# Performance work log

Hardware: AMD Instinct MI355X
Metric: run time of the kernel (lower is better)

## Reference

```python
import jax, jax.numpy as jnp
import numpy as np

SIZE = 8192
NB = 64            # nr_blocks
BS = SIZE // NB    # block_size = 128
NTOK = 4096


def setup_inputs() -> dict:
    key = jax.random.key(0)
    k1, k2, k3, k4 = jax.random.split(key, 4)
    # kaiming_normal on [nb, bs, bs]: fan_in per torch default for 3D is bs*bs? torch
    # kaiming_normal_ uses fan_in = bs (last dim sizes); we just use std=sqrt(2/BS).
    std = np.sqrt(2.0 / BS).astype(np.float32)
    x = jax.random.normal(k1, (NTOK, SIZE), dtype=jnp.float32)
    w1 = jax.random.normal(k2, (NB, BS, BS), dtype=jnp.float32) * std
    w2 = jax.random.normal(k3, (NB, BS, BS), dtype=jnp.float32) * std
    bias = jax.random.uniform(k4, (SIZE,), dtype=jnp.float32, minval=-1.0, maxval=1.0) * np.sqrt(1.0 / SIZE).astype(np.float32)
    return {"x": x, "w1": w1, "w2": w2, "bias": bias}


def _monarch(x, w1, w2, bias):
    B = x.reshape(-1, SIZE).shape[0]
    z = x.reshape(B, NB, BS)
    # first block-diagonal matmul: per-block [B,BS] @ [BS,BS]
    h = jnp.einsum('bkc,kcd->bkd', z, w1)            # [B, NB, BS]
    # Permute(size, NB): (B, NB, BS) -> (B, BS, NB) flattened
    h = h.transpose(0, 2, 1).reshape(B, NB, BS)      # regroup into NB blocks of BS
    # second block-diagonal matmul
    h = jnp.einsum('bkc,kcd->bkd', h, w2)            # [B, NB, BS]
    # Permute(size, BS): reshape (B, BS, NB) -> transpose -> (B, NB, BS)
    h = h.reshape(B, BS, NB).transpose(0, 2, 1)
    return h.reshape(x.shape) + bias


def reference(x, w1, w2, bias):
    return _monarch(x, w1, w2, bias)
```

## Files before the change

kernel.cpp:

```cpp
#include <hip/hip_runtime.h>

#define SZ 8192
#define WT_BYTES ((size_t)128 * 16384 * 2)

typedef short short8 __attribute__((ext_vector_type(8)));
typedef float f32x4 __attribute__((ext_vector_type(4)));

static __device__ __forceinline__ unsigned short f2bf(float f){
    unsigned u = __float_as_uint(f);
    u += 0x7fffu + ((u >> 16) & 1u);
    return (unsigned short)(u >> 16);
}

__global__ __launch_bounds__(256) void Monarch_prep(const float* __restrict__ w1,
                                                    const float* __restrict__ w2,
                                                    unsigned short* __restrict__ wt)
{
    __shared__ unsigned short T[128][132];
    int blk = blockIdx.x;
    const float* src = (blk < 64) ? (w1 + (size_t)blk * 16384)
                                  : (w2 + (size_t)(blk - 64) * 16384);
    unsigned short* dst = wt + (size_t)blk * 16384;
    int i  = threadIdx.x;
    int cs = i >> 5;
    int p0 = (i & 31) * 4;
    for (int rr = 0; rr < 16; ++rr){
        int c = rr * 8 + cs;
        f32x4 v = *(const f32x4*)(src + c * 128 + p0);
        T[p0 + 0][c] = f2bf(v[0]);
        T[p0 + 1][c] = f2bf(v[1]);
        T[p0 + 2][c] = f2bf(v[2]);
        T[p0 + 3][c] = f2bf(v[3]);
    }
    __syncthreads();
    for (int rr = 0; rr < 16; ++rr){
        int d = rr * 8 + cs;
        ushort4 o;
        o.x = T[d][p0 + 0]; o.y = T[d][p0 + 1]; o.z = T[d][p0 + 2]; o.w = T[d][p0 + 3];
        *(ushort4*)(dst + d * 128 + p0) = o;
    }
}

__global__ __launch_bounds__(512, 4) void Monarch_main(const float* __restrict__ x,
                                                       const unsigned short* __restrict__ w1T,
                                                       const unsigned short* __restrict__ w2T,
                                                       const float* __restrict__ bias,
                                                       float* __restrict__ out)
{
    __shared__ __align__(16) unsigned short s[16 * 2048];

    int b     = blockIdx.x;
    int xcd   = b & 7;
    int local = b >> 3;
    int g     = local & 3;
    int tile  = (xcd << 5) | (local >> 2);
    int t0    = tile << 4;
    int k0    = g << 4;
    int d0    = g << 5;

    int tid = threadIdx.x;
    int w   = tid >> 6;
    int l   = tid & 63;
    int m   = l & 15;
    int q   = l >> 4;

    const float* xrow = x + (size_t)(t0 + m) * SZ + q * 8;
    for (int jt = 0; jt < 8; ++jt){
        int j = (jt << 3) | w;
        f32x4 acc0 = {0.f, 0.f, 0.f, 0.f};
        f32x4 acc1 = {0.f, 0.f, 0.f, 0.f};
        const float* xp = xrow + j * 128;
        const unsigned short* w1p = w1T + ((size_t)(j * 128 + d0 + m)) * 128 + q * 8;
        #pragma unroll
        for (int ko = 0; ko < 4; ++ko){
            f32x4 xa = *(const f32x4*)(xp + ko * 32);
            f32x4 xb = *(const f32x4*)(xp + ko * 32 + 4);
            short8 a;
            a[0] = (short)f2bf(xa[0]); a[1] = (short)f2bf(xa[1]);
            a[2] = (short)f2bf(xa[2]); a[3] = (short)f2bf(xa[3]);
            a[4] = (short)f2bf(xb[0]); a[5] = (short)f2bf(xb[1]);
            a[6] = (short)f2bf(xb[2]); a[7] = (short)f2bf(xb[3]);
            short8 b0 = *(const short8*)(w1p + ko * 32);
            short8 b1 = *(const short8*)(w1p + 16 * 128 + ko * 32);
            acc0 = __builtin_amdgcn_mfma_f32_16x16x32_bf16(a, b0, acc0, 0, 0, 0);
            acc1 = __builtin_amdgcn_mfma_f32_16x16x32_bf16(a, b1, acc1, 0, 0, 0);
        }
        #pragma unroll
        for (int nt = 0; nt < 2; ++nt){
            int dl = nt * 16 + m;
            int gc = 8 * dl + jt;
            #pragma unroll
            for (int r = 0; r < 4; ++r){
                int t   = q * 4 + r;
                int gcs = gc ^ ((gc >> 3) & 7) ^ (t & 7);
                float v = nt ? acc1[r] : acc0[r];
                s[t * 2048 + gcs * 8 + w] = f2bf(v);
            }
        }
    }
    __syncthreads();

    f32x4 acc[2][8];
    #pragma unroll
    for (int ki = 0; ki < 2; ++ki)
        #pragma unroll
        for (int nt = 0; nt < 8; ++nt)
            acc[ki][nt] = (f32x4){0.f, 0.f, 0.f, 0.f};

    #pragma unroll
    for (int ki = 0; ki < 2; ++ki){
        int kl = w + (ki << 3);
        const unsigned short* w2p = w2T + ((size_t)((k0 + kl) * 128 + m)) * 128 + q * 8;
        #pragma unroll
        for (int ko = 0; ko < 4; ++ko){
            int gc  = kl * 16 + ko * 4 + q;
            int gcs = gc ^ ((gc >> 3) & 7) ^ (m & 7);
            short8 a = *(const short8*)(s + m * 2048 + gcs * 8);
            #pragma unroll
            for (int nt = 0; nt < 8; ++nt){
                short8 bb = *(const short8*)(w2p + nt * 16 * 128 + ko * 32);
                acc[ki][nt] = __builtin_amdgcn_mfma_f32_16x16x32_bf16(a, bb, acc[ki][nt], 0, 0, 0);
            }
        }
    }
    __syncthreads();

    float* osb = (float*)s;
    for (int h = 0; h < 2; ++h){
        if ((q >> 1) == h){
            int tb = (q & 1) * 4;
            #pragma unroll
            for (int ki = 0; ki < 2; ++ki){
                int kl = w + (ki << 3);
                #pragma unroll
                for (int nt = 0; nt < 8; ++nt){
                    int n    = nt * 16 + m;
                    int colc = (n & 63) * 32 + 2 * kl + (n >> 6);
                    int gnum = colc >> 2;
                    #pragma unroll
                    for (int r = 0; r < 4; ++r){
                        int t  = tb + r;
                        int gs = gnum ^ ((gnum >> 3) & 7) ^ (t & 7);
                        osb[t * 2048 + gs * 4 + (colc & 3)] = acc[ki][nt][r];
                    }
                }
            }
        }
        __syncthreads();
        {
            int tr = tid >> 6;
            int cl = tid & 63;
            size_t orow = (size_t)(t0 + 8 * h + tr) * SZ;
            #pragma unroll
            for (int f = 0; f < 8; ++f){
                int colc = cl * 4 + f * 256;
                int gnum = colc >> 2;
                int gs   = gnum ^ ((gnum >> 3) & 7) ^ (tr & 7);
                f32x4 v  = *(const f32x4*)(osb + tr * 2048 + gs * 4);
                int gcol = ((colc >> 5) << 7) + (g << 5) + (colc & 31);
                f32x4 bi = *(const f32x4*)(bias + gcol);
                *(f32x4*)(out + orow + gcol) = v + bi;
            }
        }
        __syncthreads();
    }
}

__global__ __launch_bounds__(256) void Monarch_fused(const float* __restrict__ x,
                                                     const float* __restrict__ w1,
                                                     const float* __restrict__ w2,
                                                     const float* __restrict__ bias,
                                                     float* __restrict__ out)
{
    __shared__ __align__(16) unsigned short s[16 * 2048];
    __shared__ __align__(16) unsigned short wst[4 * 5120];

    int b    = blockIdx.x;
    int g    = (b & 7) >> 1;
    int tile = ((b >> 3) << 1) | (b & 1);
    int t0   = tile << 4;
    int k0   = g << 4;
    int d0   = g << 5;

    int tid = threadIdx.x;
    int w   = tid >> 6;
    int l   = tid & 63;
    int m   = l & 15;
    int q   = l >> 4;

    unsigned short* wb = wst + w * 5120;
    int srow = l >> 3;
    int dcol = (l & 7) * 4;

    const float* xrow = x + (size_t)(t0 + m) * SZ + q * 8;
    for (int jt = 0; jt < 16; ++jt){
        int j = (jt << 2) | w;
        const float* wsrc = w1 + (size_t)j * 16384 + d0;
        #pragma unroll
        for (int rr = 0; rr < 16; ++rr){
            int c = rr * 8 + srow;
            f32x4 v = *(const f32x4*)(wsrc + c * 128 + dcol);
            #pragma unroll
            for (int i2 = 0; i2 < 4; ++i2)
                wb[(dcol + i2) * 136 + c] = (unsigned short)(__float_as_uint(v[i2]) >> 16);
        }
        f32x4 acc0 = {0.f, 0.f, 0.f, 0.f};
        f32x4 acc1 = {0.f, 0.f, 0.f, 0.f};
        const float* xp = xrow + j * 128;
        #pragma unroll
        for (int ko = 0; ko < 4; ++ko){
            f32x4 xa = *(const f32x4*)(xp + ko * 32);
            f32x4 xb = *(const f32x4*)(xp + ko * 32 + 4);
            short8 a;
            a[0] = (short)f2bf(xa[0]); a[1] = (short)f2bf(xa[1]);
            a[2] = (short)f2bf(xa[2]); a[3] = (short)f2bf(xa[3]);
            a[4] = (short)f2bf(xb[0]); a[5] = (short)f2bf(xb[1]);
            a[6] = (short)f2bf(xb[2]); a[7] = (short)f2bf(xb[3]);
            short8 b0 = *(const short8*)(wb + m * 136 + ko * 32 + q * 8);
            short8 b1 = *(const short8*)(wb + (m + 16) * 136 + ko * 32 + q * 8);
            acc0 = __builtin_amdgcn_mfma_f32_16x16x32_bf16(a, b0, acc0, 0, 0, 0);
            acc1 = __builtin_amdgcn_mfma_f32_16x16x32_bf16(a, b1, acc1, 0, 0, 0);
        }
        #pragma unroll
        for (int nt = 0; nt < 2; ++nt){
            int dl = nt * 16 + m;
            int gc = 8 * dl + (j >> 3);
            #pragma unroll
            for (int r = 0; r < 4; ++r){
                int t   = q * 4 + r;
                int gcs = gc ^ ((gc >> 3) & 7) ^ (t & 7);
                float v = nt ? acc1[r] : acc0[r];
                s[t * 2048 + gcs * 8 + (j & 7)] = f2bf(v);
            }
        }
    }
    __syncthreads();

    f32x4 acc[4][8];
    #pragma unroll
    for (int ki = 0; ki < 4; ++ki)
        #pragma unroll
        for (int nt = 0; nt < 8; ++nt)
            acc[ki][nt] = (f32x4){0.f, 0.f, 0.f, 0.f};

    for (int ki = 0; ki < 4; ++ki){
        int kl = w + (ki << 2);
        const float* w2src = w2 + (size_t)(k0 + kl) * 16384;
        #pragma unroll
        for (int ko = 0; ko < 4; ++ko){
            #pragma unroll
            for (int it = 0; it < 4; ++it){
                int cc = it * 8 + srow;
                const float* rp = w2src + (size_t)(ko * 32 + cc) * 128 + (l & 7) * 16;
                #pragma unroll
                for (int v4 = 0; v4 < 4; ++v4){
                    f32x4 v = *(const f32x4*)(rp + v4 * 4);
                    #pragma unroll
                    for (int i2 = 0; i2 < 4; ++i2)
                        wb[((l & 7) * 16 + v4 * 4 + i2) * 40 + cc] =
                            (unsigned short)(__float_as_uint(v[i2]) >> 16);
                }
            }
            int gc  = kl * 16 + ko * 4 + q;
            int gcs = gc ^ ((gc >> 3) & 7) ^ (m & 7);
            short8 a = *(const short8*)(s + m * 2048 + gcs * 8);
            #pragma unroll
            for (int nt = 0; nt < 8; ++nt){
                short8 bb = *(const short8*)(wb + (nt * 16 + m) * 40 + q * 8);
                acc[ki][nt] = __builtin_amdgcn_mfma_f32_16x16x32_bf16(a, bb, acc[ki][nt], 0, 0, 0);
            }
        }
    }
    __syncthreads();

    float* osb = (float*)s;
    for (int h = 0; h < 2; ++h){
        if ((q >> 1) == h){
            int tb = (q & 1) * 4;
            #pragma unroll
            for (int ki = 0; ki < 4; ++ki){
                int kl = w + (ki << 2);
                #pragma unroll
                for (int nt = 0; nt < 8; ++nt){
                    int n    = nt * 16 + m;
                    int colc = (n & 63) * 32 + 2 * kl + (n >> 6);
                    int gnum = colc >> 2;
                    #pragma unroll
                    for (int r = 0; r < 4; ++r){
                        int t  = tb + r;
                        int gs = gnum ^ ((gnum >> 3) & 7) ^ (t & 7);
                        osb[t * 2048 + gs * 4 + (colc & 3)] = acc[ki][nt][r];
                    }
                }
            }
        }
        __syncthreads();
        {
            int tr = tid >> 5;
            int cl = tid & 31;
            size_t orow = (size_t)(t0 + 8 * h + tr) * SZ;
            #pragma unroll
            for (int f = 0; f < 16; ++f){
                int colc = cl * 4 + f * 128;
                int gnum = colc >> 2;
                int gs   = gnum ^ ((gnum >> 3) & 7) ^ (tr & 7);
                f32x4 v  = *(const f32x4*)(osb + tr * 2048 + gs * 4);
                int gcol = ((colc >> 5) << 7) + (g << 5) + (colc & 31);
                f32x4 bi = *(const f32x4*)(bias + gcol);
                *(f32x4*)(out + orow + gcol) = v + bi;
            }
        }
        __syncthreads();
    }
}

extern "C" void kernel_launch(void* const* d_in, const int* in_sizes, int n_in,
                              void* d_out, int out_size, void* d_ws, size_t ws_size,
                              hipStream_t stream) {
    (void)in_sizes; (void)n_in; (void)out_size;
    const float* x    = (const float*)d_in[0];
    const float* w1   = (const float*)d_in[1];
    const float* w2   = (const float*)d_in[2];
    const float* bias = (const float*)d_in[3];

    if (ws_size >= WT_BYTES) {
        unsigned short* wt = (unsigned short*)d_ws;
        Monarch_prep<<<dim3(128), dim3(256), 0, stream>>>(w1, w2, wt);
        Monarch_main<<<dim3(1024), dim3(512), 0, stream>>>(x, wt, wt + (size_t)64 * 16384,
                                                           bias, (float*)d_out);
    } else {
        Monarch_fused<<<dim3(1024), dim3(256), 0, stream>>>(x, w1, w2, bias, (float*)d_out);
    }
}
```

Baseline: 376.3 us.

## Process 32 tokens per block to reuse weight fragments across two row tiles

Each workgroup of Monarch_main now handles 32 tokens instead of 16, so every w1/w2 fragment loaded from global memory feeds two MFMAs, one per 16-row half. The grid is halved to 512 blocks, shared memory doubles to 128 KB, and the accumulator count doubles, so the occupancy hint drops from 4 to 2 blocks per CU. The aim is to cut weight-load traffic per token. The costs are higher register and LDS pressure and fewer blocks in flight to hide the latency of the fp32 x loads.

```diff
diff --git a/kernel.cpp b/kernel.cpp
--- a/kernel.cpp
+++ b/kernel.cpp
@@ -41,20 +41,20 @@
     }
 }
 
-__global__ __launch_bounds__(512, 4) void Monarch_main(const float* __restrict__ x,
+__global__ __launch_bounds__(512, 2) void Monarch_main(const float* __restrict__ x,
                                                        const unsigned short* __restrict__ w1T,
                                                        const unsigned short* __restrict__ w2T,
                                                        const float* __restrict__ bias,
                                                        float* __restrict__ out)
 {
-    __shared__ __align__(16) unsigned short s[16 * 2048];
+    __shared__ __align__(16) unsigned short s[32 * 2048];
 
     int b     = blockIdx.x;
     int xcd   = b & 7;
     int local = b >> 3;
     int g     = local & 3;
-    int tile  = (xcd << 5) | (local >> 2);
-    int t0    = tile << 4;
+    int tgrp  = (xcd << 4) | (local >> 2);
+    int t0    = tgrp << 5;
     int k0    = g << 4;
     int d0    = g << 5;
 
@@ -64,48 +64,60 @@
     int m   = l & 15;
     int q   = l >> 4;
 
-    const float* xrow = x + (size_t)(t0 + m) * SZ + q * 8;
+    const float* xrow0 = x + (size_t)(t0 + m) * SZ + q * 8;
+    const float* xrow1 = xrow0 + (size_t)16 * SZ;
     for (int jt = 0; jt < 8; ++jt){
         int j = (jt << 3) | w;
-        f32x4 acc0 = {0.f, 0.f, 0.f, 0.f};
-        f32x4 acc1 = {0.f, 0.f, 0.f, 0.f};
-        const float* xp = xrow + j * 128;
+        f32x4 acc00 = {0.f,0.f,0.f,0.f}, acc01 = {0.f,0.f,0.f,0.f};
+        f32x4 acc10 = {0.f,0.f,0.f,0.f}, acc11 = {0.f,0.f,0.f,0.f};
+        const float* xp0 = xrow0 + j * 128;
+        const float* xp1 = xrow1 + j * 128;
         const unsigned short* w1p = w1T + ((size_t)(j * 128 + d0 + m)) * 128 + q * 8;
         #pragma unroll
         for (int ko = 0; ko < 4; ++ko){
-            f32x4 xa = *(const f32x4*)(xp + ko * 32);
-            f32x4 xb = *(const f32x4*)(xp + ko * 32 + 4);
-            short8 a;
-            a[0] = (short)f2bf(xa[0]); a[1] = (short)f2bf(xa[1]);
-            a[2] = (short)f2bf(xa[2]); a[3] = (short)f2bf(xa[3]);
-            a[4] = (short)f2bf(xb[0]); a[5] = (short)f2bf(xb[1]);
-            a[6] = (short)f2bf(xb[2]); a[7] = (short)f2bf(xb[3]);
             short8 b0 = *(const short8*)(w1p + ko * 32);
             short8 b1 = *(const short8*)(w1p + 16 * 128 + ko * 32);
-            acc0 = __builtin_amdgcn_mfma_f32_16x16x32_bf16(a, b0, acc0, 0, 0, 0);
-            acc1 = __builtin_amdgcn_mfma_f32_16x16x32_bf16(a, b1, acc1, 0, 0, 0);
-        }
-        #pragma unroll
-        for (int nt = 0; nt < 2; ++nt){
-            int dl = nt * 16 + m;
-            int gc = 8 * dl + jt;
-            #pragma unroll
-            for (int r = 0; r < 4; ++r){
-                int t   = q * 4 + r;
-                int gcs = gc ^ ((gc >> 3) & 7) ^ (t & 7);
-                float v = nt ? acc1[r] : acc0[r];
-                s[t * 2048 + gcs * 8 + w] = f2bf(v);
-            }
-        }
-    }
-    __syncthreads();
-
-    f32x4 acc[2][8];
+            f32x4 xa0 = *(const f32x4*)(xp0 + ko * 32);
+            f32x4 xb0 = *(const f32x4*)(xp0 + ko * 32 + 4);
+            f32x4 xa1 = *(const f32x4*)(xp1 + ko * 32);
+            f32x4 xb1 = *(const f32x4*)(xp1 + ko * 32 + 4);
+            short8 a0, a1;
+            a0[0] = (short)f2bf(xa0[0]); a0[1] = (short)f2bf(xa0[1]);
+            a0[2] = (short)f2bf(xa0[2]); a0[3] = (short)f2bf(xa0[3]);
+            a0[4] = (short)f2bf(xb0[0]); a0[5] = (short)f2bf(xb0[1]);
+            a0[6] = (short)f2bf(xb0[2]); a0[7] = (short)f2bf(xb0[3]);
+            a1[0] = (short)f2bf(xa1[0]); a1[1] = (short)f2bf(xa1[1]);
+            a1[2] = (short)f2bf(xa1[2]); a1[3] = (short)f2bf(xa1[3]);
+            a1[4] = (short)f2bf(xb1[0]); a1[5] = (short)f2bf(xb1[1]);
+            a1[6] = (short)f2bf(xb1[2]); a1[7] = (short)f2bf(xb1[3]);
+            acc00 = __builtin_amdgcn_mfma_f32_16x16x32_bf16(a0, b0, acc00, 0, 0, 0);
+            acc01 = __builtin_amdgcn_mfma_f32_16x16x32_bf16(a0, b1, acc01, 0, 0, 0);
+            acc10 = __builtin_amdgcn_mfma_f32_16x16x32_bf16(a1, b0, acc10, 0, 0, 0);
+            acc11 = __builtin_amdgcn_mfma_f32_16x16x32_bf16(a1, b1, acc11, 0, 0, 0);
+        }
+        #pragma unroll
+        for (int r = 0; r < 4; ++r){
+            int t   = q * 4 + r;
+            int gc0 = 8 * m + jt;
+            int gc1 = 8 * (16 + m) + jt;
+            int gcs0 = gc0 ^ ((gc0 >> 3) & 7) ^ (t & 7);
+            int gcs1 = gc1 ^ ((gc1 >> 3) & 7) ^ (t & 7);
+            s[t * 2048 + gcs0 * 8 + w]        = f2bf(acc00[r]);
+            s[t * 2048 + gcs1 * 8 + w]        = f2bf(acc01[r]);
+            s[(t + 16) * 2048 + gcs0 * 8 + w] = f2bf(acc10[r]);
+            s[(t + 16) * 2048 + gcs1 * 8 + w] = f2bf(acc11[r]);
+        }
+    }
+    __syncthreads();
+
+    f32x4 acc[2][2][8];
     #pragma unroll
     for (int ki = 0; ki < 2; ++ki)
         #pragma unroll
-        for (int nt = 0; nt < 8; ++nt)
-            acc[ki][nt] = (f32x4){0.f, 0.f, 0.f, 0.f};
+        for (int u = 0; u < 2; ++u)
+            #pragma unroll
+            for (int nt = 0; nt < 8; ++nt)
+                acc[ki][u][nt] = (f32x4){0.f, 0.f, 0.f, 0.f};
 
     #pragma unroll
     for (int ki = 0; ki < 2; ++ki){
@@ -115,54 +127,60 @@
         for (int ko = 0; ko < 4; ++ko){
             int gc  = kl * 16 + ko * 4 + q;
             int gcs = gc ^ ((gc >> 3) & 7) ^ (m & 7);
-            short8 a = *(const short8*)(s + m * 2048 + gcs * 8);
+            short8 a0 = *(const short8*)(s + m * 2048 + gcs * 8);
+            short8 a1 = *(const short8*)(s + (m + 16) * 2048 + gcs * 8);
             #pragma unroll
             for (int nt = 0; nt < 8; ++nt){
                 short8 bb = *(const short8*)(w2p + nt * 16 * 128 + ko * 32);
-                acc[ki][nt] = __builtin_amdgcn_mfma_f32_16x16x32_bf16(a, bb, acc[ki][nt], 0, 0, 0);
+                acc[ki][0][nt] = __builtin_amdgcn_mfma_f32_16x16x32_bf16(a0, bb, acc[ki][0][nt], 0, 0, 0);
+                acc[ki][1][nt] = __builtin_amdgcn_mfma_f32_16x16x32_bf16(a1, bb, acc[ki][1][nt], 0, 0, 0);
             }
         }
     }
     __syncthreads();
 
     float* osb = (float*)s;
-    for (int h = 0; h < 2; ++h){
-        if ((q >> 1) == h){
-            int tb = (q & 1) * 4;
-            #pragma unroll
-            for (int ki = 0; ki < 2; ++ki){
-                int kl = w + (ki << 3);
+    #pragma unroll
+    for (int u = 0; u < 2; ++u){
+        #pragma unroll
+        for (int h = 0; h < 2; ++h){
+            if ((q >> 1) == h){
+                int tb = (q & 1) * 4;
                 #pragma unroll
-                for (int nt = 0; nt < 8; ++nt){
-                    int n    = nt * 16 + m;
-                    int colc = (n & 63) * 32 + 2 * kl + (n >> 6);
-                    int gnum = colc >> 2;
+                for (int ki = 0; ki < 2; ++ki){
+                    int kl = w + (ki << 3);
                     #pragma unroll
-                    for (int r = 0; r < 4; ++r){
-                        int t  = tb + r;
-                        int gs = gnum ^ ((gnum >> 3) & 7) ^ (t & 7);
-                        osb[t * 2048 + gs * 4 + (colc & 3)] = acc[ki][nt][r];
+                    for (int nt = 0; nt < 8; ++nt){
+                        int n    = nt * 16 + m;
+                        int colc = (n & 63) * 32 + 2 * kl + (n >> 6);
+                        int gnum = colc >> 2;
+                        #pragma unroll
+                        for (int r = 0; r < 4; ++r){
+                            int t  = tb + r;
+                            int gs = gnum ^ ((gnum >> 3) & 7) ^ (t & 7);
+                            osb[t * 2048 + gs * 4 + (colc & 3)] = acc[ki][u][nt][r];
+                        }
                     }
                 }
             }
-        }
-        __syncthreads();
-        {
-            int tr = tid >> 6;
-            int cl = tid & 63;
-            size_t orow = (size_t)(t0 + 8 * h + tr) * SZ;
-            #pragma unroll
-            for (int f = 0; f < 8; ++f){
-                int colc = cl * 4 + f * 256;
-                int gnum = colc >> 2;
-                int gs   = gnum ^ ((gnum >> 3) & 7) ^ (tr & 7);
-                f32x4 v  = *(const f32x4*)(osb + tr * 2048 + gs * 4);
-                int gcol = ((colc >> 5) << 7) + (g << 5) + (colc & 31);
-                f32x4 bi = *(const f32x4*)(bias + gcol);
-                *(f32x4*)(out + orow + gcol) = v + bi;
-            }
-        }
-        __syncthreads();
+            __syncthreads();
+            {
+                int tr = tid >> 6;
+                int cl = tid & 63;
+                size_t orow = (size_t)(t0 + u * 16 + 8 * h + tr) * SZ;
+                #pragma unroll
+                for (int f = 0; f < 8; ++f){
+                    int colc = cl * 4 + f * 256;
+                    int gnum = colc >> 2;
+                    int gs   = gnum ^ ((gnum >> 3) & 7) ^ (tr & 7);
+                    f32x4 v  = *(const f32x4*)(osb + tr * 2048 + gs * 4);
+                    int gcol = ((colc >> 5) << 7) + (g << 5) + (colc & 31);
+                    f32x4 bi = *(const f32x4*)(bias + gcol);
+                    *(f32x4*)(out + orow + gcol) = v + bi;
+                }
+            }
+            __syncthreads();
+        }
     }
 }
 
@@ -326,8 +344,8 @@
     if (ws_size >= WT_BYTES) {
         unsigned short* wt = (unsigned short*)d_ws;
         Monarch_prep<<<dim3(128), dim3(256), 0, stream>>>(w1, w2, wt);
-        Monarch_main<<<dim3(1024), dim3(512), 0, stream>>>(x, wt, wt + (size_t)64 * 16384,
-                                                           bias, (float*)d_out);
+        Monarch_main<<<dim3(512), dim3(512), 0, stream>>>(x, wt, wt + (size_t)64 * 16384,
+                                                          bias, (float*)d_out);
     } else {
         Monarch_fused<<<dim3(1024), dim3(256), 0, stream>>>(x, w1, w2, bias, (float*)d_out);
     }
```

Result: faster. 321.6 us (-14.5%).
